# Performance work log

Hardware: AMD Instinct MI355X
Metric: run time of the kernel (lower is better)

Reference implementation:

```python
import jax, jax.numpy as jnp
import numpy as np

N, DIM = 8192, 128
NEG = -1e9  # finite stand-in for -inf; exp underflows to 0 for masked entries


def setup_inputs() -> dict:
    key = jax.random.key(0)
    k1, k2, k3, k4 = jax.random.split(key, 4)
    h = jax.random.normal(k1, (N, DIM), dtype=jnp.float32)
    social_adj = jax.random.randint(k2, (N, N), 0, 2, dtype=jnp.int32)
    # nn.Linear(dim, dim, bias=False): weight [out, in]; xavier-ish scale
    W = jax.random.normal(k3, (DIM, DIM), dtype=jnp.float32) / np.sqrt(DIM)
    a = jax.random.normal(k4, (2 * DIM,), dtype=jnp.float32) / np.sqrt(2 * DIM)
    return {"h": h, "social_adj": social_adj, "W": W, "a": a}


def reference(h, social_adj, W, a):
    Wh = h @ W.T                              # [N, d]
    d = Wh.shape[1]
    a1 = Wh @ a[:d]                           # [N]
    a2 = Wh @ a[d:]                           # [N]
    e = jax.nn.leaky_relu(a1[:, None] + a2[None, :], negative_slope=0.2)  # [N, N]
    mask = social_adj != 0
    e = jnp.where(mask, e, NEG)
    alpha = jax.nn.softmax(e, axis=-1)        # [N, N]
    # rows with no neighbors: torch gives nan->0 via nan_to_num; we zero them directly
    no_neighbor = ~jnp.any(mask, axis=-1)     # [N]
    alpha = jnp.where(no_neighbor[:, None], 0.0, alpha)
    out = alpha @ Wh                          # [N, d]; already 0 on no_neighbor rows
    return out, alpha
```

## Files before the change

kernel.cpp:

```cpp
#include <hip/hip_runtime.h>
#include <hip/hip_bf16.h>

#define NN 8192
#define DIM 128
#define KS 8
#define KSL (NN / KS)
#define RPB 64
#define KC 128

typedef __attribute__((ext_vector_type(8))) short bf16x8;
typedef __attribute__((ext_vector_type(4))) float f32x4;
typedef __attribute__((ext_vector_type(4))) int i32x4;
typedef __attribute__((ext_vector_type(4))) unsigned int u32x4;
typedef __attribute__((ext_vector_type(4))) unsigned short u16x4;
typedef __attribute__((ext_vector_type(4))) short s16x4;

static __device__ inline unsigned short f2bf(float x) {
    __hip_bfloat16 b = __float2bfloat16(x);
    return *reinterpret_cast<unsigned short*>(&b);
}

struct BSplit { short hi, lo; };
static __device__ inline BSplit bsplit(float x) {
    BSplit r;
    __hip_bfloat16 h = __float2bfloat16(x);
    r.hi = *reinterpret_cast<short*>(&h);
    float rem = x - __bfloat162float(h);
    __hip_bfloat16 l = __float2bfloat16(rem);
    r.lo = *reinterpret_cast<short*>(&l);
    return r;
}

__global__ __launch_bounds__(256) void k1m(const float* __restrict__ h,
                                           const float* __restrict__ W,
                                           const float* __restrict__ a,
                                           __hip_bfloat16* __restrict__ whbT,
                                           float* __restrict__ a1g,
                                           float2* __restrict__ pk) {
    __shared__ short whi[128 * 132];
    __shared__ short wlo[128 * 132];
    __shared__ short wt[8 * 128 * 8];
    __shared__ float a_sh[256];

    const int tid = threadIdx.x;
    const int wv = tid >> 6, lane = tid & 63;
    const int r0 = blockIdx.x * 64;

    for (int idx = tid; idx < 128 * 128; idx += 256) {
        const int d = idx >> 7, k = idx & 127;
        BSplit s = bsplit(W[idx]);
        whi[d * 132 + k] = s.hi;
        wlo[d * 132 + k] = s.lo;
    }
    a_sh[tid] = a[tid];
    __syncthreads();

    f32x4 acc[8];
    #pragma unroll
    for (int n = 0; n < 8; ++n) acc[n] = (f32x4){0.f, 0.f, 0.f, 0.f};

    const int arow = r0 + wv * 16 + (lane & 15);
    const int ksub = (lane >> 4) * 8;
    const float* hp = h + (size_t)arow * DIM + ksub;

    #pragma unroll
    for (int kk = 0; kk < 128; kk += 32) {
        f32x4 x0 = *(const f32x4*)(hp + kk);
        f32x4 x1 = *(const f32x4*)(hp + kk + 4);
        bf16x8 ah, al;
        {
            BSplit s0 = bsplit(x0.x), s1 = bsplit(x0.y), s2 = bsplit(x0.z), s3 = bsplit(x0.w);
            BSplit s4 = bsplit(x1.x), s5 = bsplit(x1.y), s6 = bsplit(x1.z), s7 = bsplit(x1.w);
            ah[0] = s0.hi; al[0] = s0.lo; ah[1] = s1.hi; al[1] = s1.lo;
            ah[2] = s2.hi; al[2] = s2.lo; ah[3] = s3.hi; al[3] = s3.lo;
            ah[4] = s4.hi; al[4] = s4.lo; ah[5] = s5.hi; al[5] = s5.lo;
            ah[6] = s6.hi; al[6] = s6.lo; ah[7] = s7.hi; al[7] = s7.lo;
        }
        #pragma unroll
        for (int n = 0; n < 8; ++n) {
            const int boff = (n * 16 + (lane & 15)) * 132 + kk + ksub;
            bf16x8 bh = *(const bf16x8*)(whi + boff);
            bf16x8 bl = *(const bf16x8*)(wlo + boff);
            acc[n] = __builtin_amdgcn_mfma_f32_16x16x32_bf16(ah, bh, acc[n], 0, 0, 0);
            acc[n] = __builtin_amdgcn_mfma_f32_16x16x32_bf16(ah, bl, acc[n], 0, 0, 0);
            acc[n] = __builtin_amdgcn_mfma_f32_16x16x32_bf16(al, bh, acc[n], 0, 0, 0);
        }
    }

    float p1[4] = {0.f, 0.f, 0.f, 0.f}, p2[4] = {0.f, 0.f, 0.f, 0.f};
    #pragma unroll
    for (int n = 0; n < 8; ++n) {
        const float av1 = a_sh[n * 16 + (lane & 15)];
        const float av2 = a_sh[128 + n * 16 + (lane & 15)];
        #pragma unroll
        for (int q = 0; q < 4; ++q) {
            p1[q] += acc[n][q] * av1;
            p2[q] += acc[n][q] * av2;
        }
    }
    #pragma unroll
    for (int o = 8; o >= 1; o >>= 1) {
        #pragma unroll
        for (int q = 0; q < 4; ++q) {
            p1[q] += __shfl_xor(p1[q], o, 64);
            p2[q] += __shfl_xor(p2[q], o, 64);
        }
    }
    if ((lane & 15) == 0) {
        #pragma unroll
        for (int q = 0; q < 4; ++q) {
            const int row = r0 + wv * 16 + (lane >> 4) * 4 + q;
            a1g[row] = p1[q];
            const float E1v = expf(p2[q]);
            const float E2v = expf(0.2f * p2[q]);
            unsigned ub = (unsigned)f2bf(E1v) | ((unsigned)f2bf(E2v) << 16);
            float2 pv;
            pv.x = p2[q];
            pv.y = __uint_as_float(ub);
            pk[row] = pv;
        }
    }

    #pragma unroll
    for (int n = 0; n < 8; ++n) {
        #pragma unroll
        for (int q = 0; q < 4; ++q) {
            const int kloc = wv * 16 + (lane >> 4) * 4 + q;
            const int d = n * 16 + (lane & 15);
            wt[(kloc >> 3) * 1024 + d * 8 + (kloc & 7)] = (short)f2bf(acc[n][q]);
        }
    }
    __syncthreads();
    short* dst = reinterpret_cast<short*>(whbT) + ((size_t)r0 << 7);
    for (int idx = tid * 4; idx < 8192; idx += 1024)
        *(s16x4*)(dst + idx) = *(const s16x4*)(wt + idx);
}

static __device__ inline void sa_group(const i32x4 v, const f32x4 pa, const f32x4 pb,
                                       const float a1i, const int lane,
                                       float& s1, float& s2,
                                       unsigned* __restrict__ bgrp) {
    unsigned long long m0 = __ballot(v.x != 0);
    unsigned long long m1 = __ballot(v.y != 0);
    unsigned long long m2 = __ballot(v.z != 0);
    unsigned long long m3 = __ballot(v.w != 0);
    if (lane == 0) {
        u32x4 w;
        w.x = (unsigned)m0; w.y = (unsigned)m1;
        w.z = (unsigned)m2; w.w = (unsigned)m3;
        *(u32x4*)(bgrp) = w;
    } else if (lane == 32) {
        u32x4 w;
        w.x = (unsigned)(m0 >> 32); w.y = (unsigned)(m1 >> 32);
        w.z = (unsigned)(m2 >> 32); w.w = (unsigned)(m3 >> 32);
        *(u32x4*)(bgrp + 4) = w;
    }
    float x2, e1, e2; unsigned ub; bool px;
    x2 = pa.x; ub = __float_as_uint(pa.y);
    e1 = __uint_as_float(ub << 16); e2 = __uint_as_float(ub & 0xffff0000u);
    px = (a1i + x2 >= 0.f);
    s1 += (v.x && px) ? e1 : 0.f;  s2 += (v.x && !px) ? e2 : 0.f;
    x2 = pa.z; ub = __float_as_uint(pa.w);
    e1 = __uint_as_float(ub << 16); e2 = __uint_as_float(ub & 0xffff0000u);
    px = (a1i + x2 >= 0.f);
    s1 += (v.y && px) ? e1 : 0.f;  s2 += (v.y && !px) ? e2 : 0.f;
    x2 = pb.x; ub = __float_as_uint(pb.y);
    e1 = __uint_as_float(ub << 16); e2 = __uint_as_float(ub & 0xffff0000u);
    px = (a1i + x2 >= 0.f);
    s1 += (v.z && px) ? e1 : 0.f;  s2 += (v.z && !px) ? e2 : 0.f;
    x2 = pb.z; ub = __float_as_uint(pb.w);
    e1 = __uint_as_float(ub << 16); e2 = __uint_as_float(ub & 0xffff0000u);
    px = (a1i + x2 >= 0.f);
    s1 += (v.w && px) ? e1 : 0.f;  s2 += (v.w && !px) ? e2 : 0.f;
}

__global__ __launch_bounds__(256) void sa_scan(const int* __restrict__ adj,
                                               const float* __restrict__ a1g,
                                               const float2* __restrict__ pk,
                                               unsigned* __restrict__ bm,
                                               float* __restrict__ crow) {
    const int wid = threadIdx.x >> 6, lane = threadIdx.x & 63;
    const int i = blockIdx.x * 4 + wid;
    const float a1i = a1g[i];
    const int* arow = adj + (size_t)i * NN;
    unsigned* brow = bm + (size_t)i * (NN / 32);
    const float* pkf = reinterpret_cast<const float*>(pk);

    float s1 = 0.f, s2 = 0.f;
    for (int it = 0; it < NN / 1024; ++it) {
        const int j0 = it * 1024 + lane * 4;
        i32x4 v0 = __builtin_nontemporal_load((const i32x4*)(arow + j0));
        i32x4 v1 = __builtin_nontemporal_load((const i32x4*)(arow + j0 + 256));
        i32x4 v2 = __builtin_nontemporal_load((const i32x4*)(arow + j0 + 512));
        i32x4 v3 = __builtin_nontemporal_load((const i32x4*)(arow + j0 + 768));
        f32x4 pa0 = *(const f32x4*)(pkf + 2 * j0);
        f32x4 pb0 = *(const f32x4*)(pkf + 2 * j0 + 4);
        f32x4 pa1 = *(const f32x4*)(pkf + 2 * (j0 + 256));
        f32x4 pb1 = *(const f32x4*)(pkf + 2 * (j0 + 256) + 4);
        f32x4 pa2 = *(const f32x4*)(pkf + 2 * (j0 + 512));
        f32x4 pb2 = *(const f32x4*)(pkf + 2 * (j0 + 512) + 4);
        f32x4 pa3 = *(const f32x4*)(pkf + 2 * (j0 + 768));
        f32x4 pb3 = *(const f32x4*)(pkf + 2 * (j0 + 768) + 4);
        unsigned* bsup = brow + it * 32;
        sa_group(v0, pa0, pb0, a1i, lane, s1, s2, bsup);
        sa_group(v1, pa1, pb1, a1i, lane, s1, s2, bsup + 8);
        sa_group(v2, pa2, pb2, a1i, lane, s1, s2, bsup + 16);
        sa_group(v3, pa3, pb3, a1i, lane, s1, s2, bsup + 24);
    }
    #pragma unroll
    for (int o = 32; o >= 1; o >>= 1) {
        s1 += __shfl_xor(s1, o, 64);
        s2 += __shfl_xor(s2, o, 64);
    }
    if (lane == 0) {
        float c1 = 0.f, c2 = 0.f;
        if (s1 + s2 > 0.f) {
            float e1v = expf(a1i);
            float e2v = expf(0.2f * a1i);
            float S = e1v * s1 + e2v * s2;
            c1 = e1v / S;
            c2 = e2v / S;
        }
        crow[i * 4 + 0] = c1;
        crow[i * 4 + 1] = c2;
        crow[i * 4 + 2] = a1i;
        crow[i * 4 + 3] = 0.f;
    }
}

__global__ __launch_bounds__(512, 8) void sb_pv(const unsigned* __restrict__ bm,
                                                const float* __restrict__ crowG,
                                                const float2* __restrict__ pk,
                                                const __hip_bfloat16* __restrict__ whbT,
                                                float* __restrict__ alpha,
                                                float* __restrict__ part) {
    __shared__ __hip_bfloat16 abuf[2][RPB][KC + 8];

    const int tid = threadIdx.x;
    const int wv = tid >> 6, lane = tid & 63;
    const int r0 = blockIdx.x * RPB;
    const int ks = blockIdx.y;
    const int k0 = ks * KSL;
    const float* pkf = reinterpret_cast<const float*>(pk);

    const int rloc = tid >> 5;
    float c1r[4], c2r[4], a1r[4];
    #pragma unroll
    for (int v = 0; v < 4; ++v) {
        f32x4 cw = *(const f32x4*)(crowG + (size_t)(r0 + rloc + 16 * v) * 4);
        c1r[v] = cw.x; c2r[v] = cw.y; a1r[v] = cw.z;
    }

    f32x4 acc[4];
    #pragma unroll
    for (int rt = 0; rt < 4; ++rt) acc[rt] = (f32x4){0.f, 0.f, 0.f, 0.f};
    const int n0 = wv * 16;
    const short* wb = reinterpret_cast<const short*>(whbT);
    const short* bbase = wb + (size_t)(n0 + (lane & 15)) * 8 + (size_t)(lane >> 4) * 1024;

    const int cgrp = (tid & 31) << 2;
    const unsigned pbit = tid & 31;

    for (int kc = 0; kc < KSL; kc += KC) {
        const int dbuf = (kc >> 7) & 1;
        const int jl = kc + cgrp;
        const int j = k0 + jl;
        const int wbw = ((jl >> 8) << 3) + (((jl >> 7) & 1) << 2);
        f32x4 pa = *(const f32x4*)(pkf + 2 * j);
        f32x4 pb = *(const f32x4*)(pkf + 2 * j + 4);
        #pragma unroll
        for (int v = 0; v < 4; ++v) {
            const int r = rloc + 16 * v;
            const int gr = r0 + r;
            u32x4 w4 = *(const u32x4*)(bm + (size_t)gr * (NN / 32) + ks * (KSL / 32) + wbw);
            const float c1 = c1r[v], c2 = c2r[v], a1i = a1r[v];
            f32x4 al;
            {
                unsigned ub = __float_as_uint(pa.y);
                float e1 = __uint_as_float(ub << 16), e2 = __uint_as_float(ub & 0xffff0000u);
                al.x = ((w4.x >> pbit) & 1) ? ((a1i + pa.x >= 0.f) ? c1 * e1 : c2 * e2) : 0.f;
            }
            {
                unsigned ub = __float_as_uint(pa.w);
                float e1 = __uint_as_float(ub << 16), e2 = __uint_as_float(ub & 0xffff0000u);
                al.y = ((w4.y >> pbit) & 1) ? ((a1i + pa.z >= 0.f) ? c1 * e1 : c2 * e2) : 0.f;
            }
            {
                unsigned ub = __float_as_uint(pb.y);
                float e1 = __uint_as_float(ub << 16), e2 = __uint_as_float(ub & 0xffff0000u);
                al.z = ((w4.z >> pbit) & 1) ? ((a1i + pb.x >= 0.f) ? c1 * e1 : c2 * e2) : 0.f;
            }
            {
                unsigned ub = __float_as_uint(pb.w);
                float e1 = __uint_as_float(ub << 16), e2 = __uint_as_float(ub & 0xffff0000u);
                al.w = ((w4.w >> pbit) & 1) ? ((a1i + pb.z >= 0.f) ? c1 * e1 : c2 * e2) : 0.f;
            }
            __builtin_nontemporal_store(al, (f32x4*)(alpha + (size_t)gr * NN + j));
            u16x4 ub4;
            ub4.x = f2bf(al.x); ub4.y = f2bf(al.y); ub4.z = f2bf(al.z); ub4.w = f2bf(al.w);
            *(u16x4*)(&abuf[dbuf][r][cgrp]) = ub4;
        }
        __syncthreads();
        #pragma unroll
        for (int kk = 0; kk < KC; kk += 32) {
            bf16x8 bf = *(const bf16x8*)(bbase + (size_t)((k0 + kc + kk) >> 3) * 1024);
            #pragma unroll
            for (int rt = 0; rt < 4; ++rt) {
                bf16x8 af = *(const bf16x8*)(&abuf[dbuf][rt * 16 + (lane & 15)][kk + 8 * (lane >> 4)]);
                acc[rt] = __builtin_amdgcn_mfma_f32_16x16x32_bf16(af, bf, acc[rt], 0, 0, 0);
            }
        }
    }

    float* pb2 = part + (size_t)ks * NN * DIM;
    const int rb = (lane >> 4) * 4;
    #pragma unroll
    for (int rt = 0; rt < 4; ++rt) {
        #pragma unroll
        for (int q = 0; q < 4; ++q)
            pb2[(size_t)(r0 + rt * 16 + rb + q) * DIM + n0 + (lane & 15)] = acc[rt][q];
    }
}

__global__ __launch_bounds__(256) void k5_reduce(const float* __restrict__ part,
                                                 float* __restrict__ out) {
    const size_t idx = ((size_t)blockIdx.x * 256 + threadIdx.x) * 4;
    f32x4 s = (f32x4){0.f, 0.f, 0.f, 0.f};
    #pragma unroll
    for (int ks = 0; ks < KS; ++ks)
        s += *(const f32x4*)(part + (size_t)ks * NN * DIM + idx);
    *(f32x4*)(out + idx) = s;
}

extern "C" void kernel_launch(void* const* d_in, const int* in_sizes, int n_in,
                              void* d_out, int out_size, void* d_ws, size_t ws_size,
                              hipStream_t stream) {
    const float* h   = (const float*)d_in[0];
    const int*   adj = (const int*)d_in[1];
    const float* W   = (const float*)d_in[2];
    const float* a   = (const float*)d_in[3];

    float* out   = (float*)d_out;
    float* alpha = out + (size_t)NN * DIM;

    char* ws = (char*)d_ws;
    __hip_bfloat16* whbT = (__hip_bfloat16*)(ws);
    float* a1g   = (float*)(ws + 0x200000);
    float2* pk   = (float2*)(ws + 0x208000);
    float* crow  = (float*)(ws + 0x218000);
    unsigned* bm = (unsigned*)(ws + 0x240000);
    float* part  = (float*)(ws + 0xA40000);

    k1m<<<NN / 64, 256, 0, stream>>>(h, W, a, whbT, a1g, pk);
    sa_scan<<<NN / 4, 256, 0, stream>>>(adj, a1g, pk, bm, crow);
    sb_pv<<<dim3(NN / RPB, KS), 512, 0, stream>>>(bm, crow, pk, whbT, alpha, part);
    k5_reduce<<<NN * DIM / 1024, 256, 0, stream>>>(part, out);
}
```

Measured before the change: 167.6 us.

## Widen K chunk to 256, single-buffer LDS, and stage row constants in shared memory

Doubles the K chunk per iteration in sb_pv to 256 columns. Each wave now handles 8 rows, with every lane covering 4 contiguous columns, so alpha stores and mask loads are wider per row. The double-buffered alpha tile becomes a single buffer plus a trailing barrier, and per-row softmax constants are read from a small shared array instead of registers. Halving the loop trip count and the pk loads per row is meant to improve store coalescing. The cost is two barriers per chunk and no overlap between the alpha-build phase and the MFMA phase.

```diff
diff --git a/kernel.cpp b/kernel.cpp
--- a/kernel.cpp
+++ b/kernel.cpp
@@ -6,7 +6,7 @@
 #define KS 8
 #define KSL (NN / KS)
 #define RPB 64
-#define KC 128
+#define KC 256
 
 typedef __attribute__((ext_vector_type(8))) short bf16x8;
 typedef __attribute__((ext_vector_type(4))) float f32x4;
@@ -234,7 +234,8 @@
                                                 const __hip_bfloat16* __restrict__ whbT,
                                                 float* __restrict__ alpha,
                                                 float* __restrict__ part) {
-    __shared__ __hip_bfloat16 abuf[2][RPB][KC + 8];
+    __shared__ __hip_bfloat16 abuf[RPB][KC + 8];
+    __shared__ float crowL[RPB][4];
 
     const int tid = threadIdx.x;
     const int wv = tid >> 6, lane = tid & 63;
@@ -243,13 +244,9 @@
     const int k0 = ks * KSL;
     const float* pkf = reinterpret_cast<const float*>(pk);
 
-    const int rloc = tid >> 5;
-    float c1r[4], c2r[4], a1r[4];
-    #pragma unroll
-    for (int v = 0; v < 4; ++v) {
-        f32x4 cw = *(const f32x4*)(crowG + (size_t)(r0 + rloc + 16 * v) * 4);
-        c1r[v] = cw.x; c2r[v] = cw.y; a1r[v] = cw.z;
-    }
+    if (tid < RPB * 4)
+        crowL[tid >> 2][tid & 3] = crowG[(r0 + (tid >> 2)) * 4 + (tid & 3)];
+    __syncthreads();
 
     f32x4 acc[4];
     #pragma unroll
@@ -258,22 +255,20 @@
     const short* wb = reinterpret_cast<const short*>(whbT);
     const short* bbase = wb + (size_t)(n0 + (lane & 15)) * 8 + (size_t)(lane >> 4) * 1024;
 
-    const int cgrp = (tid & 31) << 2;
-    const unsigned pbit = tid & 31;
+    const unsigned pbit = lane & 31;
 
     for (int kc = 0; kc < KSL; kc += KC) {
-        const int dbuf = (kc >> 7) & 1;
-        const int jl = kc + cgrp;
-        const int j = k0 + jl;
-        const int wbw = ((jl >> 8) << 3) + (((jl >> 7) & 1) << 2);
+        const int j = k0 + kc + lane * 4;
         f32x4 pa = *(const f32x4*)(pkf + 2 * j);
         f32x4 pb = *(const f32x4*)(pkf + 2 * j + 4);
-        #pragma unroll
-        for (int v = 0; v < 4; ++v) {
-            const int r = rloc + 16 * v;
+        const int wbase = (kc >> 5) + (lane >> 5) * 4;
+        #pragma unroll
+        for (int v = 0; v < 8; ++v) {
+            const int r = v * 8 + wv;
             const int gr = r0 + r;
-            u32x4 w4 = *(const u32x4*)(bm + (size_t)gr * (NN / 32) + ks * (KSL / 32) + wbw);
-            const float c1 = c1r[v], c2 = c2r[v], a1i = a1r[v];
+            u32x4 w4 = *(const u32x4*)(bm + (size_t)gr * (NN / 32) + ks * (KSL / 32) + wbase);
+            f32x4 cw = *(const f32x4*)(&crowL[r][0]);
+            const float c1 = cw.x, c2 = cw.y, a1i = cw.z;
             f32x4 al;
             {
                 unsigned ub = __float_as_uint(pa.y);
@@ -298,7 +293,7 @@
             __builtin_nontemporal_store(al, (f32x4*)(alpha + (size_t)gr * NN + j));
             u16x4 ub4;
             ub4.x = f2bf(al.x); ub4.y = f2bf(al.y); ub4.z = f2bf(al.z); ub4.w = f2bf(al.w);
-            *(u16x4*)(&abuf[dbuf][r][cgrp]) = ub4;
+            *(u16x4*)(&abuf[r][lane * 4]) = ub4;
         }
         __syncthreads();
         #pragma unroll
@@ -306,10 +301,11 @@
             bf16x8 bf = *(const bf16x8*)(bbase + (size_t)((k0 + kc + kk) >> 3) * 1024);
             #pragma unroll
             for (int rt = 0; rt < 4; ++rt) {
-                bf16x8 af = *(const bf16x8*)(&abuf[dbuf][rt * 16 + (lane & 15)][kk + 8 * (lane >> 4)]);
+                bf16x8 af = *(const bf16x8*)(&abuf[rt * 16 + (lane & 15)][kk + 8 * (lane >> 4)]);
                 acc[rt] = __builtin_amdgcn_mfma_f32_16x16x32_bf16(af, bf, acc[rt], 0, 0, 0);
             }
         }
+        __syncthreads();
     }
 
     float* pb2 = part + (size_t)ks * NN * DIM;
```

New measurement: 177.5 us. +5.9%, slower.
